# Kernel optimization log

Hardware: AMD Instinct MI355X
Metric: run time of the kernel (lower is better)

The kernel has to match this reference:

```python
import jax, jax.numpy as jnp
import numpy as np

B, N, C, H, D, K = 4, 8192, 384, 12, 2, 256
M = N // K          # 32 members per cluster
CH = C // H         # 32 head dim


def setup_inputs() -> dict:
    key = jax.random.key(0)
    ks = jax.random.split(key, 8)
    pos = jax.random.uniform(ks[0], (B, N, D), jnp.float32) * 100.0
    feat = jax.random.normal(ks[1], (B, N, C), jnp.float32)
    # each batch's points partitioned into K clusters of M members (a permutation)
    perms = jax.vmap(lambda kk: jax.random.permutation(kk, N))(jax.random.split(ks[2], B))
    member_idx = perms.reshape(B * K, M).astype(jnp.int32)               # z x m
    batch_idx = jnp.broadcast_to(
        jnp.repeat(jnp.arange(B, dtype=jnp.int32), K)[:, None], (B * K, M))
    w = 0.02
    qkv_w = jax.random.normal(ks[3], (3 * C, C), jnp.float32) * w
    qkv_b = jnp.zeros((3 * C,), jnp.float32)
    pos_w = jax.random.normal(ks[4], (H, D), jnp.float32) * w
    pos_b = jnp.zeros((H,), jnp.float32)
    proj_w = jax.random.normal(ks[5], (C, C), jnp.float32) * w
    proj_b = jnp.zeros((C,), jnp.float32)
    return dict(pos=pos, feat=feat, member_idx=member_idx, batch_idx=batch_idx,
                qkv_w=qkv_w, qkv_b=qkv_b, pos_w=pos_w, pos_b=pos_b,
                proj_w=proj_w, proj_b=proj_b, k=K)


def reference(pos, feat, member_idx, batch_idx, qkv_w, qkv_b, pos_w, pos_b,
              proj_w, proj_b, k):
    # attend_means=True, mask=None, cluster_score=None, q_subsample_idx=None path
    b, n, c = feat.shape
    d = pos.shape[2]
    h = pos_w.shape[0]
    ch = c // h
    z, m = member_idx.shape
    scale = ch ** -0.5

    qkv = feat @ qkv_w.T + qkv_b            # b,n,3c
    q = qkv[..., :c]                        # b,n,c
    kv = qkv[..., c:]                       # b,n,2c

    pos_orig = pos
    pos_n = pos / jnp.max(pos.reshape(-1, d), axis=0)   # per-coordinate max norm

    # irregular gather of kv / pos per cluster member
    kv_g = kv[batch_idx, member_idx]        # z,m,2c
    pos_g = pos_n[batch_idx, member_idx]    # z,m,d

    # cluster_score=None, mask=None -> uniform weights 1/m (mean over members)
    kv_mean = jnp.mean(kv_g, axis=1).reshape(b, k, 2, h, ch)
    pos_mean = jnp.mean(pos_g, axis=1).reshape(b, k, d)

    key_ = kv_mean[:, :, 0].transpose(0, 2, 1, 3)   # b,h,k,ch
    v = kv_mean[:, :, 1].transpose(0, 2, 1, 3)      # b,h,k,ch
    qh = q.reshape(b, n, h, ch).transpose(0, 2, 1, 3) * scale  # b,h,n,ch

    attn = jnp.einsum('bhnc,bhkc->bhnk', qh, key_)  # b,h,n,k
    rel_pos = pos_mean[:, None, :, :] - pos_orig[:, :, None, :]  # b,n,k,d
    pos_bias = jnp.einsum('bnkd,hd->bhnk', rel_pos, pos_w) + pos_b[None, :, None, None]
    attn = jax.nn.softmax(attn + pos_bias, axis=-1)

    out = jnp.einsum('bhnk,bhkc->bnhc', attn, v).reshape(b, n, c)
    return out @ proj_w.T + proj_b
```

## Files before the change

### kernel.cpp

```cpp
#include <hip/hip_runtime.h>

typedef __attribute__((ext_vector_type(8))) short bf16x8;
typedef __attribute__((ext_vector_type(4))) float f32x4;

#define MFMA16(a,b,c) __builtin_amdgcn_mfma_f32_16x16x32_bf16((a),(b),(c),0,0,0)

__device__ __forceinline__ float b2f(unsigned short u){
  union { unsigned u; float f; } x; x.u = ((unsigned)u) << 16; return x.f;
}
__device__ __forceinline__ unsigned short f2b(float f){
  union { float f; unsigned u; } x; x.f = f;
  unsigned r = x.u + 0x7FFFu + ((x.u >> 16) & 1u);
  return (unsigned short)(r >> 16);
}
__device__ __forceinline__ unsigned pk_rne(float a, float b){
  unsigned ua = __float_as_uint(a), ub = __float_as_uint(b);
  ua += 0x7FFFu + ((ua >> 16) & 1u);
  ub += 0x7FFFu + ((ub >> 16) & 1u);
  return __builtin_amdgcn_perm(ub, ua, 0x07060302u);
}
__device__ __forceinline__ unsigned pk_trunc(float a, float b){
  return __builtin_amdgcn_perm(__float_as_uint(b), __float_as_uint(a), 0x07060302u);
}
__device__ __forceinline__ bf16x8 mk8(unsigned a, unsigned b, unsigned c, unsigned d){
  union { uint4 u; bf16x8 h; } x; x.u = make_uint4(a,b,c,d); return x.h;
}
__device__ __forceinline__ int permp(int cl){
  return (cl & 0xE0) | (((cl >> 2) & 3) << 3) | (((cl >> 4) & 1) << 2) | (cl & 3);
}

typedef __attribute__((address_space(3))) unsigned int lds_u32;
typedef const __attribute__((address_space(1))) unsigned int glb_u32;
__device__ __forceinline__ void gl_lds16(const void* g, void* l){
  __builtin_amdgcn_global_load_lds((glb_u32*)g, (lds_u32*)l, 16, 0, 0);
}

__global__ __launch_bounds__(192) void prep_means_kernel(
    const float* __restrict__ pos, unsigned* __restrict__ pmax,
    const float* __restrict__ qkv_w, unsigned short* __restrict__ qkvwb,
    const float* __restrict__ proj_w, unsigned short* __restrict__ projwb,
    const float* __restrict__ feat,
    const int* __restrict__ member_idx, const int* __restrict__ batch_idx,
    unsigned short* __restrict__ fm, float* __restrict__ pm,
    unsigned short* __restrict__ featb)
{
  int bid = blockIdx.x, t = threadIdx.x;
  if (bid < 1024){
    int g = t / 96, tl = t - g*96;
    int z = bid;
    __shared__ int bases[32];
    __shared__ float4 part[96];
    if (t < 32) bases[t] = batch_idx[z*32 + t]*8192 + member_idx[z*32 + t];
    __syncthreads();
    if (t < 32){
      float2 pp = ((const float2*)pos)[bases[t]];
      #pragma unroll
      for (int off = 16; off >= 1; off >>= 1){
        pp.x += __shfl_xor(pp.x, off, 32);
        pp.y += __shfl_xor(pp.y, off, 32);
      }
      if (t == 0){ pm[z*2] = pp.x*(1.f/32.f); pm[z*2+1] = pp.y*(1.f/32.f); }
    }
    float4 v[16]; int rows[16];
    const float4* f4 = (const float4*)feat;
    #pragma unroll
    for (int m = 0; m < 16; m++){
      rows[m] = bases[g*16 + m];
      v[m] = f4[(long)rows[m]*96 + tl];
    }
    float4 a = {0.f,0.f,0.f,0.f};
    #pragma unroll
    for (int m = 0; m < 16; m++){
      *(uint2*)(featb + (long)rows[m]*384 + tl*4) =
          make_uint2(pk_rne(v[m].x, v[m].y), pk_rne(v[m].z, v[m].w));
      a.x += v[m].x; a.y += v[m].y; a.z += v[m].z; a.w += v[m].w;
    }
    if (g == 1) part[tl] = a;
    __syncthreads();
    if (g == 0){
      float4 b = part[tl];
      a.x += b.x; a.y += b.y; a.z += b.z; a.w += b.w;
      unsigned d0 = pk_rne(a.x*(1.f/32.f), a.y*(1.f/32.f));
      unsigned d1 = pk_rne(a.z*(1.f/32.f), a.w*(1.f/32.f));
      *(uint2*)(fm + (long)z*384 + tl*4) = make_uint2(d0, d1);
    }
  } else if (bid < 1408){
    int u = (bid - 1024)*192 + t;
    const float* in; unsigned short* o; long i;
    if (u < 55296){ in = qkv_w;  o = qkvwb;  i = u; }
    else          { in = proj_w; o = projwb; i = u - 55296; }
    const float4* p = (const float4*)(in + i*8);
    float4 a = p[0], b = p[1];
    *(uint4*)(o + i*8) = make_uint4(pk_rne(a.x,a.y), pk_rne(a.z,a.w),
                                    pk_rne(b.x,b.y), pk_rne(b.z,b.w));
  } else {
    int i = (bid - 1408)*192 + t;
    if (i < 16384){
      float4 v = ((const float4*)pos)[i];
      float m0 = fmaxf(v.x, v.z), m1 = fmaxf(v.y, v.w);
      #pragma unroll
      for (int off = 32; off >= 1; off >>= 1){
        m0 = fmaxf(m0, __shfl_xor(m0, off, 64));
        m1 = fmaxf(m1, __shfl_xor(m1, off, 64));
      }
      if ((t & 63) == 0){
        atomicMax(&pmax[0], __float_as_uint(m0));
        atomicMax(&pmax[1], __float_as_uint(m1));
      }
    }
  }
}

__global__ __launch_bounds__(512) void kvq_kernel(
    const unsigned short* __restrict__ fm,
    const unsigned short* __restrict__ featb,
    const unsigned short* __restrict__ qkvwb,
    const float* __restrict__ qkv_b,
    const float* __restrict__ pm, const float* __restrict__ pmaxf,
    const float* __restrict__ pos_w, const float* __restrict__ pos_b,
    unsigned short* __restrict__ kh, unsigned short* __restrict__ vt,
    unsigned short* __restrict__ wt,
    unsigned short* __restrict__ q_s, float q_scale)
{
  __shared__ unsigned short As[64*64];
  __shared__ unsigned short Ws[384*64];
  __shared__ unsigned short wtS[256];
  const int K = 384;
  int tid = threadIdx.x;
  int lane = tid & 63, wave = tid >> 6;
  int l15 = lane & 15, quad = lane >> 4;
  int sw = l15 & 7;
  int srow = tid >> 3, sc8 = tid & 7;

  int qtile;
  if (blockIdx.x < 96){
    int mt = blockIdx.x / 6, nt = blockIdx.x - mt*6;
    int m0 = mt << 6, n0 = nt << 7;
    int b = m0 >> 8, cl0 = m0 & 255;
    const unsigned short* W = qkvwb + 384*384;
    if (nt >= 3 && tid < 256){
      int lh = tid >> 6, lc = tid & 63;
      int h = ((n0 - 384) >> 5) + lh;
      int cl = cl0 + lc;
      float p0 = pm[(b*256 + cl)*2]   / pmaxf[0];
      float p1 = pm[(b*256 + cl)*2+1] / pmaxf[1];
      float bias = p0*pos_w[h*2] + p1*pos_w[h*2+1] + pos_b[h];
      unsigned short wv = f2b(exp2f(bias * 1.44269504088896340f));
      wtS[lh*64 + lc] = wv;
      wt[(((long)(b*12 + h)) << 8) + permp(cl)] = wv;
    }
    int wr = (wave >> 2) << 5, wc = (wave & 3) << 5;
    f32x4 acc[2][2];
    #pragma unroll
    for (int i = 0; i < 2; i++)
      #pragma unroll
      for (int j = 0; j < 2; j++) acc[i][j] = (f32x4){0.f,0.f,0.f,0.f};

    for (int k0 = 0; k0 < K; k0 += 64){
      __syncthreads();
      int gc8 = sc8 ^ (srow & 7);
      gl_lds16(fm + (long)(m0+srow)*K + k0 + gc8*8, As + wave*512);
      #pragma unroll
      for (int it = 0; it < 2; it++){
        int r = it*64 + srow;
        int g2 = sc8 ^ (r & 7);
        gl_lds16(W + (long)(n0+r)*K + k0 + g2*8, Ws + it*4096 + wave*512);
      }
      __syncthreads();
      #pragma unroll
      for (int kk = 0; kk < 2; kk++){
        bf16x8 af[2], bfr[2];
        #pragma unroll
        for (int i = 0; i < 2; i++)
          af[i] = *(const bf16x8*)(As + (wr + i*16 + l15)*64 + (((kk<<2)+quad) ^ sw)*8);
        #pragma unroll
        for (int j = 0; j < 2; j++)
          bfr[j] = *(const bf16x8*)(Ws + (wc + j*16 + l15)*64 + (((kk<<2)+quad) ^ sw)*8);
        #pragma unroll
        for (int i = 0; i < 2; i++)
          #pragma unroll
          for (int j = 0; j < 2; j++)
            acc[i][j] = MFMA16(af[i], bfr[j], acc[i][j]);
      }
    }

    #pragma unroll
    for (int j = 0; j < 2; j++){
      int col = n0 + wc + j*16 + l15;
      float bv = qkv_b[384 + col];
      #pragma unroll
      for (int i = 0; i < 2; i++){
        #pragma unroll
        for (int r = 0; r < 4; r++){
          float v = acc[i][j][r] + bv;
          int lr = wr + i*16 + quad*4 + r;
          int cl = cl0 + lr;
          if (col < 384){
            int h = col >> 5, ch = col & 31;
            kh[((((long)b*12 + h)*256 + cl)*32) + ch] = f2b(v);
          } else {
            int cn = col - 384;
            int h = cn >> 5, ch = cn & 31;
            int pp = permp(cl);
            int c8 = (pp >> 3) ^ (ch & 7);
            float w = b2f(wtS[(wave & 3)*64 + lr]);
            vt[(((long)b*12 + h)*32 + ch)*256 + c8*8 + (pp & 7)] = f2b(v * w);
          }
        }
      }
    }
    qtile = 416 + blockIdx.x;
  } else {
    qtile = blockIdx.x - 96;
  }

  {
    int m0 = qtile << 6;
    f32x4 acc[4][3];
    #pragma unroll
    for (int i = 0; i < 4; i++)
      #pragma unroll
      for (int j = 0; j < 3; j++) acc[i][j] = (f32x4){0.f,0.f,0.f,0.f};

    for (int k0 = 0; k0 < K; k0 += 64){
      __syncthreads();
      int gc8 = sc8 ^ (srow & 7);
      gl_lds16(featb + (long)(m0+srow)*K + k0 + gc8*8, As + wave*512);
      #pragma unroll
      for (int it = 0; it < 6; it++){
        int r = it*64 + srow;
        int g2 = sc8 ^ (r & 7);
        gl_lds16(qkvwb + (long)r*K + k0 + g2*8, Ws + it*4096 + wave*512);
      }
      __syncthreads();
      #pragma unroll
      for (int kk = 0; kk < 2; kk++){
        bf16x8 af[4];
        #pragma unroll
        for (int i = 0; i < 4; i++)
          af[i] = *(const bf16x8*)(As + (i*16 + l15)*64 + (((kk<<2)+quad) ^ sw)*8);
        #pragma unroll
        for (int j = 0; j < 3; j++){
          bf16x8 bfr = *(const bf16x8*)(Ws + (wave*48 + j*16 + l15)*64 + (((kk<<2)+quad) ^ sw)*8);
          #pragma unroll
          for (int i = 0; i < 4; i++)
            acc[i][j] = MFMA16(af[i], bfr, acc[i][j]);
        }
      }
    }

    #pragma unroll
    for (int j = 0; j < 3; j++){
      int col = wave*48 + j*16 + l15;
      float bv = qkv_b[col];
      #pragma unroll
      for (int i = 0; i < 4; i++){
        int row0 = m0 + i*16 + quad*4;
        #pragma unroll
        for (int r = 0; r < 4; r++){
          float v = (acc[i][j][r] + bv) * q_scale;
          int row = row0 + r;
          int bb = row >> 13, tok = row & 8191;
          q_s[((((long)(bb*12 + (col >> 5))) << 13) + tok)*32 + (col & 31)] = f2b(v);
        }
      }
    }
  }
}

__global__ __launch_bounds__(512) void gemm_proj_kernel(
    const unsigned short* __restrict__ A, const unsigned short* __restrict__ W,
    const float* __restrict__ bias, float* __restrict__ C)
{
  __shared__ unsigned short As[64*64];
  __shared__ unsigned short Ws[384*64];
  const int K = 384, N = 384;
  int m0 = blockIdx.x << 6;
  int tid = threadIdx.x;
  int lane = tid & 63, wave = tid >> 6;
  int l15 = lane & 15, quad = lane >> 4;
  int sw = l15 & 7;
  int srow = tid >> 3, sc8 = tid & 7;

  f32x4 acc[4][3];
  #pragma unroll
  for (int i = 0; i < 4; i++)
    #pragma unroll
    for (int j = 0; j < 3; j++) acc[i][j] = (f32x4){0.f,0.f,0.f,0.f};

  for (int k0 = 0; k0 < K; k0 += 64){
    __syncthreads();
    {
      int gc8 = sc8 ^ (srow & 7);
      int row = m0 + srow;
      int bb = row >> 13, tok = row & 8191;
      int ch = k0 + gc8*8;
      const unsigned short* asrc = A + ((((long)(bb*12 + (ch >> 5))) << 13) + tok)*32 + (ch & 31);
      gl_lds16(asrc, As + wave*512);
    }
    #pragma unroll
    for (int it = 0; it < 6; it++){
      int r = it*64 + srow;
      int g2 = sc8 ^ (r & 7);
      gl_lds16(W + (long)r*K + k0 + g2*8, Ws + it*4096 + wave*512);
    }
    __syncthreads();
    #pragma unroll
    for (int kk = 0; kk < 2; kk++){
      bf16x8 af[4];
      #pragma unroll
      for (int i = 0; i < 4; i++)
        af[i] = *(const bf16x8*)(As + (i*16 + l15)*64 + (((kk<<2)+quad) ^ sw)*8);
      #pragma unroll
      for (int j = 0; j < 3; j++){
        bf16x8 bfr = *(const bf16x8*)(Ws + (wave*48 + j*16 + l15)*64 + (((kk<<2)+quad) ^ sw)*8);
        #pragma unroll
        for (int i = 0; i < 4; i++)
          acc[i][j] = MFMA16(af[i], bfr, acc[i][j]);
      }
    }
  }

  #pragma unroll
  for (int j = 0; j < 3; j++){
    int col = wave*48 + j*16 + l15;
    float bv = bias[col];
    #pragma unroll
    for (int i = 0; i < 4; i++){
      int row0 = m0 + i*16 + quad*4;
      #pragma unroll
      for (int r = 0; r < 4; r++)
        C[(long)(row0 + r)*N + col] = acc[i][j][r] + bv;
    }
  }
}

__global__ __launch_bounds__(256) void attn_kernel(
    const unsigned short* __restrict__ qhm,
    const unsigned short* __restrict__ kh,
    const unsigned short* __restrict__ vt,
    const unsigned short* __restrict__ wt,
    unsigned short* __restrict__ aohm)
{
  __shared__ unsigned short keyS[256*32];
  __shared__ unsigned short vTS[32*256];
  __shared__ unsigned short wS[256];

  int bid = blockIdx.x;
  int chunk = bid & 31;
  int bh = bid >> 5;
  int n0 = chunk << 8;
  int tid = threadIdx.x, lane = tid & 63, wave = tid >> 6;
  int l15 = lane & 15, quad = lane >> 4;
  int sw = l15 & 7;

  const unsigned short* khb = kh + (long)bh*8192;
  const unsigned short* vtb = vt + (long)bh*8192;
  #pragma unroll
  for (int it = 0; it < 4; it++){
    gl_lds16(khb + it*2048 + tid*8, keyS + it*2048 + wave*512);
    gl_lds16(vtb + it*2048 + tid*8, vTS  + it*2048 + wave*512);
  }
  if (tid < 32) *(uint4*)(wS + tid*8) = *(const uint4*)(wt + ((long)bh << 8) + tid*8);

  long qbase = ((long)bh*8192 + n0 + wave*64 + l15)*32 + quad*8;
  bf16x8 aq[4];
  #pragma unroll
  for (int ti = 0; ti < 4; ti++)
    aq[ti] = *(const bf16x8*)(qhm + qbase + ti*512);
  __syncthreads();

  f32x4 o0[4], o1[4], os[4];
  #pragma unroll
  for (int ti = 0; ti < 4; ti++){
    o0[ti] = (f32x4){0.f,0.f,0.f,0.f};
    o1[ti] = (f32x4){0.f,0.f,0.f,0.f};
    os[ti] = (f32x4){0.f,0.f,0.f,0.f};
  }

  #pragma unroll
  for (int ks = 0; ks < 8; ks++){
    bf16x8 bk0 = *(const bf16x8*)(keyS + ((2*ks  )*16 + l15)*32 + quad*8);
    bf16x8 bk1 = *(const bf16x8*)(keyS + ((2*ks+1)*16 + l15)*32 + quad*8);
    const f32x4 z4 = {0.f,0.f,0.f,0.f};
    bf16x8 pf[4];
    #pragma unroll
    for (int ti = 0; ti < 4; ti++){
      f32x4 s0 = MFMA16(bk0, aq[ti], z4);
      f32x4 s1 = MFMA16(bk1, aq[ti], z4);
      #pragma unroll
      for (int c = 0; c < 4; c++){ s0[c] = exp2f(s0[c]); s1[c] = exp2f(s1[c]); }
      pf[ti] = mk8(pk_trunc(s0[0],s0[1]), pk_trunc(s0[2],s0[3]),
                   pk_trunc(s1[0],s1[1]), pk_trunc(s1[2],s1[3]));
    }
    int c8 = (4*ks + quad) ^ sw;
    bf16x8 a0 = *(const bf16x8*)(vTS + l15*256      + c8*8);
    bf16x8 a1 = *(const bf16x8*)(vTS + (16+l15)*256 + c8*8);
    bf16x8 wf = *(const bf16x8*)(wS + ks*32 + quad*8);
    #pragma unroll
    for (int ti = 0; ti < 4; ti++){
      o0[ti] = MFMA16(a0, pf[ti], o0[ti]);
      o1[ti] = MFMA16(a1, pf[ti], o1[ti]);
      os[ti] = MFMA16(wf, pf[ti], os[ti]);
    }
  }

  #pragma unroll
  for (int ti = 0; ti < 4; ti++){
    float inv = 1.f / os[ti][0];
    long ob = ((long)bh*8192 + n0 + wave*64 + ti*16 + l15)*32 + quad*4;
    *(uint2*)(aohm + ob)      = make_uint2(pk_rne(o0[ti][0]*inv, o0[ti][1]*inv),
                                           pk_rne(o0[ti][2]*inv, o0[ti][3]*inv));
    *(uint2*)(aohm + ob + 16) = make_uint2(pk_rne(o1[ti][0]*inv, o1[ti][1]*inv),
                                           pk_rne(o1[ti][2]*inv, o1[ti][3]*inv));
  }
}

extern "C" void kernel_launch(void* const* d_in, const int* in_sizes, int n_in,
                              void* d_out, int out_size, void* d_ws, size_t ws_size,
                              hipStream_t stream)
{
  const float* pos      = (const float*)d_in[0];
  const float* feat     = (const float*)d_in[1];
  const int* member_idx = (const int*)d_in[2];
  const int* batch_idx  = (const int*)d_in[3];
  const float* qkv_w    = (const float*)d_in[4];
  const float* qkv_b    = (const float*)d_in[5];
  const float* pos_w    = (const float*)d_in[6];
  const float* pos_b    = (const float*)d_in[7];
  const float* proj_w   = (const float*)d_in[8];
  const float* proj_b   = (const float*)d_in[9];
  float* out = (float*)d_out;

  char* ws = (char*)d_ws;
  float* pmax           = (float*)ws;
  float* pm             = (float*)(ws + 256);
  unsigned short* fm    = (unsigned short*)(ws + 8704);
  unsigned short* kh    = (unsigned short*)(ws + 795136);
  unsigned short* vt    = (unsigned short*)(ws + 1581568);
  unsigned short* wt    = (unsigned short*)(ws + 2368000);
  unsigned short* q_s   = (unsigned short*)(ws + 2417152);
  unsigned short* ao    = (unsigned short*)(ws + 27582976);
  unsigned short* qkvwb = (unsigned short*)(ws + 52748800);
  unsigned short* projwb= (unsigned short*)(ws + 53633536);
  unsigned short* featb = (unsigned short*)(ws + 53928448);

  hipMemsetAsync(pmax, 0, 8, stream);
  prep_means_kernel<<<1494, 192, 0, stream>>>(pos, (unsigned*)pmax, qkv_w, qkvwb,
                                              proj_w, projwb, feat, member_idx,
                                              batch_idx, fm, pm, featb);
  kvq_kernel<<<512, 512, 0, stream>>>(fm, featb, qkvwb, qkv_b, pm, pmax, pos_w, pos_b,
                                      kh, vt, wt, q_s,
                                      0.17677669529663687f * 1.44269504088896340f);
  attn_kernel<<<1536, 256, 0, stream>>>(q_s, kh, vt, wt, ao);
  gemm_proj_kernel<<<512, 512, 0, stream>>>(ao, projwb, proj_b, out);
}
```

Before: 186.8 us.

## Fuse cluster attention with output projection into one kernel

Merges the attention kernel and the projection GEMM into a single kernel. Each block handles 64 tokens of one batch, loops over head pairs, computes the attention output into LDS, and immediately accumulates it against the projection weights. This removes the bf16 attention-output round trip through global memory and one kernel launch. In exchange, key/value tiles are reloaded per block (each block now covers all heads for only 64 tokens), projection weights are read straight from global memory without LDS staging, and there are extra barriers per head pair.

New measurement: 186.4 us. About the same (-0.2%).

```diff
diff --git a/kernel.cpp b/kernel.cpp
--- a/kernel.cpp
+++ b/kernel.cpp
@@ -268,151 +268,113 @@
   }
 }
 
-__global__ __launch_bounds__(512) void gemm_proj_kernel(
-    const unsigned short* __restrict__ A, const unsigned short* __restrict__ W,
-    const float* __restrict__ bias, float* __restrict__ C)
-{
-  __shared__ unsigned short As[64*64];
-  __shared__ unsigned short Ws[384*64];
-  const int K = 384, N = 384;
-  int m0 = blockIdx.x << 6;
-  int tid = threadIdx.x;
-  int lane = tid & 63, wave = tid >> 6;
-  int l15 = lane & 15, quad = lane >> 4;
-  int sw = l15 & 7;
-  int srow = tid >> 3, sc8 = tid & 7;
-
-  f32x4 acc[4][3];
-  #pragma unroll
-  for (int i = 0; i < 4; i++)
-    #pragma unroll
-    for (int j = 0; j < 3; j++) acc[i][j] = (f32x4){0.f,0.f,0.f,0.f};
-
-  for (int k0 = 0; k0 < K; k0 += 64){
-    __syncthreads();
-    {
-      int gc8 = sc8 ^ (srow & 7);
-      int row = m0 + srow;
-      int bb = row >> 13, tok = row & 8191;
-      int ch = k0 + gc8*8;
-      const unsigned short* asrc = A + ((((long)(bb*12 + (ch >> 5))) << 13) + tok)*32 + (ch & 31);
-      gl_lds16(asrc, As + wave*512);
-    }
-    #pragma unroll
-    for (int it = 0; it < 6; it++){
-      int r = it*64 + srow;
-      int g2 = sc8 ^ (r & 7);
-      gl_lds16(W + (long)r*K + k0 + g2*8, Ws + it*4096 + wave*512);
-    }
-    __syncthreads();
-    #pragma unroll
-    for (int kk = 0; kk < 2; kk++){
-      bf16x8 af[4];
-      #pragma unroll
-      for (int i = 0; i < 4; i++)
-        af[i] = *(const bf16x8*)(As + (i*16 + l15)*64 + (((kk<<2)+quad) ^ sw)*8);
-      #pragma unroll
-      for (int j = 0; j < 3; j++){
-        bf16x8 bfr = *(const bf16x8*)(Ws + (wave*48 + j*16 + l15)*64 + (((kk<<2)+quad) ^ sw)*8);
-        #pragma unroll
-        for (int i = 0; i < 4; i++)
-          acc[i][j] = MFMA16(af[i], bfr, acc[i][j]);
-      }
-    }
-  }
-
-  #pragma unroll
-  for (int j = 0; j < 3; j++){
-    int col = wave*48 + j*16 + l15;
-    float bv = bias[col];
-    #pragma unroll
-    for (int i = 0; i < 4; i++){
-      int row0 = m0 + i*16 + quad*4;
-      #pragma unroll
-      for (int r = 0; r < 4; r++)
-        C[(long)(row0 + r)*N + col] = acc[i][j][r] + bv;
-    }
-  }
-}
-
-__global__ __launch_bounds__(256) void attn_kernel(
+__global__ __launch_bounds__(512, 4) void attnproj_kernel(
     const unsigned short* __restrict__ qhm,
     const unsigned short* __restrict__ kh,
     const unsigned short* __restrict__ vt,
     const unsigned short* __restrict__ wt,
-    unsigned short* __restrict__ aohm)
+    const unsigned short* __restrict__ projwb,
+    const float* __restrict__ proj_b,
+    float* __restrict__ out)
 {
-  __shared__ unsigned short keyS[256*32];
-  __shared__ unsigned short vTS[32*256];
-  __shared__ unsigned short wS[256];
+  __shared__ unsigned short keyS[16384];
+  __shared__ unsigned short vTS[16384];
+  __shared__ unsigned short oS[64*64];
+  __shared__ unsigned short wS[512];
 
   int bid = blockIdx.x;
-  int chunk = bid & 31;
-  int bh = bid >> 5;
-  int n0 = chunk << 8;
+  int b = bid >> 7;
+  int t0 = (bid & 127) << 6;
   int tid = threadIdx.x, lane = tid & 63, wave = tid >> 6;
   int l15 = lane & 15, quad = lane >> 4;
   int sw = l15 & 7;
-
-  const unsigned short* khb = kh + (long)bh*8192;
-  const unsigned short* vtb = vt + (long)bh*8192;
+  int hsel = wave >> 2, ti = wave & 3;
+
+  f32x4 acc[4][3];
   #pragma unroll
-  for (int it = 0; it < 4; it++){
-    gl_lds16(khb + it*2048 + tid*8, keyS + it*2048 + wave*512);
-    gl_lds16(vtb + it*2048 + tid*8, vTS  + it*2048 + wave*512);
+  for (int i = 0; i < 4; i++)
+    #pragma unroll
+    for (int j = 0; j < 3; j++) acc[i][j] = (f32x4){0.f,0.f,0.f,0.f};
+
+  for (int it = 0; it < 6; it++){
+    int h0 = 2*it;
+    const unsigned short* ks = kh + ((long)b*12 + h0)*8192;
+    const unsigned short* vs = vt + ((long)b*12 + h0)*8192;
+    #pragma unroll
+    for (int p = 0; p < 4; p++){
+      gl_lds16(ks + p*4096 + tid*8, keyS + p*4096 + wave*512);
+      gl_lds16(vs + p*4096 + tid*8, vTS  + p*4096 + wave*512);
+    }
+    if (wave == 0)
+      gl_lds16(wt + ((long)b*12 + h0)*256 + lane*8, wS);
+
+    long bh = (long)b*12 + h0 + hsel;
+    bf16x8 aq = *(const bf16x8*)(qhm + (bh*8192 + t0 + ti*16 + l15)*32 + quad*8);
+    __syncthreads();
+
+    const unsigned short* kb = keyS + hsel*8192;
+    const unsigned short* vb = vTS  + hsel*8192;
+    const unsigned short* wb = wS   + hsel*256;
+
+    f32x4 o0 = {0.f,0.f,0.f,0.f}, o1 = {0.f,0.f,0.f,0.f}, os = {0.f,0.f,0.f,0.f};
+    #pragma unroll
+    for (int ks8 = 0; ks8 < 8; ks8++){
+      bf16x8 bk0 = *(const bf16x8*)(kb + ((2*ks8  )*16 + l15)*32 + quad*8);
+      bf16x8 bk1 = *(const bf16x8*)(kb + ((2*ks8+1)*16 + l15)*32 + quad*8);
+      const f32x4 z4 = {0.f,0.f,0.f,0.f};
+      f32x4 s0 = MFMA16(bk0, aq, z4);
+      f32x4 s1 = MFMA16(bk1, aq, z4);
+      #pragma unroll
+      for (int c = 0; c < 4; c++){ s0[c] = exp2f(s0[c]); s1[c] = exp2f(s1[c]); }
+      bf16x8 pf = mk8(pk_trunc(s0[0],s0[1]), pk_trunc(s0[2],s0[3]),
+                      pk_trunc(s1[0],s1[1]), pk_trunc(s1[2],s1[3]));
+      int c8 = (4*ks8 + quad) ^ sw;
+      bf16x8 a0 = *(const bf16x8*)(vb + l15*256      + c8*8);
+      bf16x8 a1 = *(const bf16x8*)(vb + (16+l15)*256 + c8*8);
+      bf16x8 wf = *(const bf16x8*)(wb + ks8*32 + quad*8);
+      o0 = MFMA16(a0, pf, o0);
+      o1 = MFMA16(a1, pf, o1);
+      os = MFMA16(wf, pf, os);
+    }
+
+    float inv = 1.f / os[0];
+    int tokLoc = ti*16 + l15;
+    int oct0 = hsel*4 + (quad >> 1);
+    int wi = (quad & 1)*4;
+    *(uint2*)(oS + tokLoc*64 + ((oct0 ^ sw)*8 + wi)) =
+        make_uint2(pk_rne(o0[0]*inv, o0[1]*inv), pk_rne(o0[2]*inv, o0[3]*inv));
+    *(uint2*)(oS + tokLoc*64 + (((oct0+2) ^ sw)*8 + wi)) =
+        make_uint2(pk_rne(o1[0]*inv, o1[1]*inv), pk_rne(o1[2]*inv, o1[3]*inv));
+    __syncthreads();
+
+    #pragma unroll
+    for (int kk = 0; kk < 2; kk++){
+      bf16x8 af[4];
+      #pragma unroll
+      for (int i = 0; i < 4; i++)
+        af[i] = *(const bf16x8*)(oS + (i*16 + l15)*64 + (((kk<<2)+quad) ^ sw)*8);
+      #pragma unroll
+      for (int j = 0; j < 3; j++){
+        bf16x8 bfr = *(const bf16x8*)(projwb + (long)(wave*48 + j*16 + l15)*384
+                                      + it*64 + (kk*4 + quad)*8);
+        #pragma unroll
+        for (int i = 0; i < 4; i++)
+          acc[i][j] = MFMA16(af[i], bfr, acc[i][j]);
+      }
+    }
   }
-  if (tid < 32) *(uint4*)(wS + tid*8) = *(const uint4*)(wt + ((long)bh << 8) + tid*8);
-
-  long qbase = ((long)bh*8192 + n0 + wave*64 + l15)*32 + quad*8;
-  bf16x8 aq[4];
+
   #pragma unroll
-  for (int ti = 0; ti < 4; ti++)
-    aq[ti] = *(const bf16x8*)(qhm + qbase + ti*512);
-  __syncthreads();
-
-  f32x4 o0[4], o1[4], os[4];
-  #pragma unroll
-  for (int ti = 0; ti < 4; ti++){
-    o0[ti] = (f32x4){0.f,0.f,0.f,0.f};
-    o1[ti] = (f32x4){0.f,0.f,0.f,0.f};
-    os[ti] = (f32x4){0.f,0.f,0.f,0.f};
-  }
-
-  #pragma unroll
-  for (int ks = 0; ks < 8; ks++){
-    bf16x8 bk0 = *(const bf16x8*)(keyS + ((2*ks  )*16 + l15)*32 + quad*8);
-    bf16x8 bk1 = *(const bf16x8*)(keyS + ((2*ks+1)*16 + l15)*32 + quad*8);
-    const f32x4 z4 = {0.f,0.f,0.f,0.f};
-    bf16x8 pf[4];
-    #pragma unroll
-    for (int ti = 0; ti < 4; ti++){
-      f32x4 s0 = MFMA16(bk0, aq[ti], z4);
-      f32x4 s1 = MFMA16(bk1, aq[ti], z4);
-      #pragma unroll
-      for (int c = 0; c < 4; c++){ s0[c] = exp2f(s0[c]); s1[c] = exp2f(s1[c]); }
-      pf[ti] = mk8(pk_trunc(s0[0],s0[1]), pk_trunc(s0[2],s0[3]),
-                   pk_trunc(s1[0],s1[1]), pk_trunc(s1[2],s1[3]));
-    }
-    int c8 = (4*ks + quad) ^ sw;
-    bf16x8 a0 = *(const bf16x8*)(vTS + l15*256      + c8*8);
-    bf16x8 a1 = *(const bf16x8*)(vTS + (16+l15)*256 + c8*8);
-    bf16x8 wf = *(const bf16x8*)(wS + ks*32 + quad*8);
-    #pragma unroll
-    for (int ti = 0; ti < 4; ti++){
-      o0[ti] = MFMA16(a0, pf[ti], o0[ti]);
-      o1[ti] = MFMA16(a1, pf[ti], o1[ti]);
-      os[ti] = MFMA16(wf, pf[ti], os[ti]);
-    }
-  }
-
-  #pragma unroll
-  for (int ti = 0; ti < 4; ti++){
-    float inv = 1.f / os[ti][0];
-    long ob = ((long)bh*8192 + n0 + wave*64 + ti*16 + l15)*32 + quad*4;
-    *(uint2*)(aohm + ob)      = make_uint2(pk_rne(o0[ti][0]*inv, o0[ti][1]*inv),
-                                           pk_rne(o0[ti][2]*inv, o0[ti][3]*inv));
-    *(uint2*)(aohm + ob + 16) = make_uint2(pk_rne(o1[ti][0]*inv, o1[ti][1]*inv),
-                                           pk_rne(o1[ti][2]*inv, o1[ti][3]*inv));
+  for (int j = 0; j < 3; j++){
+    int col = wave*48 + j*16 + l15;
+    float bv = proj_b[col];
+    #pragma unroll
+    for (int i = 0; i < 4; i++){
+      long row0 = (long)b*8192 + t0 + i*16 + quad*4;
+      #pragma unroll
+      for (int r = 0; r < 4; r++)
+        out[(row0 + r)*384 + col] = acc[i][j][r] + bv;
+    }
   }
 }
 
@@ -440,7 +402,6 @@
   unsigned short* vt    = (unsigned short*)(ws + 1581568);
   unsigned short* wt    = (unsigned short*)(ws + 2368000);
   unsigned short* q_s   = (unsigned short*)(ws + 2417152);
-  unsigned short* ao    = (unsigned short*)(ws + 27582976);
   unsigned short* qkvwb = (unsigned short*)(ws + 52748800);
   unsigned short* projwb= (unsigned short*)(ws + 53633536);
   unsigned short* featb = (unsigned short*)(ws + 53928448);
@@ -452,6 +413,5 @@
   kvq_kernel<<<512, 512, 0, stream>>>(fm, featb, qkvwb, qkv_b, pm, pmax, pos_w, pos_b,
                                       kh, vt, wt, q_s,
                                       0.17677669529663687f * 1.44269504088896340f);
-  attn_kernel<<<1536, 256, 0, stream>>>(q_s, kh, vt, wt, ao);
-  gemm_proj_kernel<<<512, 512, 0, stream>>>(ao, projwb, proj_b, out);
-}
+  attnproj_kernel<<<512, 512, 0, stream>>>(q_s, kh, vt, wt, projwb, proj_b, out);
+}
```
